# Kernel tuning notes

Measured on AMD Instinct MI355X. Metric: run time of the kernel, lower is better.

Reference implementation:

```python
import jax, jax.numpy as jnp
import numpy as np

HIDDEN = 2048
NUM_HEADS = 16
HEAD_DIM = HIDDEN // NUM_HEADS
INTER = 8192
EPS = 1e-6


def setup_inputs() -> dict:
    key = jax.random.key(0)
    ks = jax.random.split(key, 10)
    s = 0.02
    return {
        "x": jax.random.normal(ks[0], (2, 2048, HIDDEN), dtype=jnp.float32),
        "w_ln1": jnp.ones((HIDDEN,), dtype=jnp.float32),
        "wq": jax.random.normal(ks[1], (HIDDEN, HIDDEN), dtype=jnp.float32) * s,
        "wk": jax.random.normal(ks[2], (HIDDEN, HIDDEN), dtype=jnp.float32) * s,
        "wv": jax.random.normal(ks[3], (HIDDEN, HIDDEN), dtype=jnp.float32) * s,
        "wo": jax.random.normal(ks[4], (HIDDEN, HIDDEN), dtype=jnp.float32) * s,
        "w_ln2": jnp.ones((HIDDEN,), dtype=jnp.float32),
        "wg": jax.random.normal(ks[5], (INTER, HIDDEN), dtype=jnp.float32) * s,
        "wu": jax.random.normal(ks[6], (INTER, HIDDEN), dtype=jnp.float32) * s,
        "wd": jax.random.normal(ks[7], (HIDDEN, INTER), dtype=jnp.float32) * s,
    }


def rmsnorm(x, w):
    rms = jnp.sqrt(jnp.mean(x * x, axis=-1, keepdims=True) + EPS)
    return x / rms * w


def attention(x, wq, wk, wv, wo):
    B, T, C = x.shape
    # weights are [out, in] (torch Linear convention) -> x @ W.T
    q = (x @ wq.T).reshape(B, T, NUM_HEADS, HEAD_DIM)
    k = (x @ wk.T).reshape(B, T, NUM_HEADS, HEAD_DIM)
    v = (x @ wv.T).reshape(B, T, NUM_HEADS, HEAD_DIM)
    scores = jnp.einsum("bqhd,bkhd->bhqk", q, k) / jnp.sqrt(jnp.float32(HEAD_DIM))
    attn = jax.nn.softmax(scores, axis=-1)
    out = jnp.einsum("bhqk,bkhd->bqhd", attn, v).reshape(B, T, C)
    return out @ wo.T


def mlp(x, wg, wu, wd):
    return (jax.nn.silu(x @ wg.T) * (x @ wu.T)) @ wd.T


def reference(x, w_ln1, wq, wk, wv, wo, w_ln2, wg, wu, wd):
    x = x + attention(rmsnorm(x, w_ln1), wq, wk, wv, wo)
    x = x + mlp(rmsnorm(x, w_ln2), wg, wu, wd)
    return x
```

## Files before the change

kernel.cpp:

```cpp
#include <hip/hip_runtime.h>
#include <stdint.h>

typedef unsigned short u16;
typedef unsigned int   u32;
typedef short s16x8 __attribute__((ext_vector_type(8)));
typedef u16   u16x8 __attribute__((ext_vector_type(8)));
typedef float f32x4 __attribute__((ext_vector_type(4)));

__device__ __forceinline__ u16 f2bf(float f) {
    u32 u = __float_as_uint(f);
    u32 r = u + 0x7fffu + ((u >> 16) & 1u);
    return (u16)(r >> 16);
}
__device__ __forceinline__ float bf2f(u16 h) {
    return __uint_as_float(((u32)h) << 16);
}

#define GLD16(gp, lp) __builtin_amdgcn_global_load_lds(                          \
    (const __attribute__((address_space(1))) void*)(uintptr_t)(gp),             \
    (__attribute__((address_space(3))) void*)(u32)(uintptr_t)(lp), 16, 0, 0)

#define FENCE asm volatile("" ::: "memory")

template<int N> __device__ __forceinline__ void waitv() {
    if constexpr (N == 0)      asm volatile("s_waitcnt vmcnt(0)" ::: "memory");
    else if constexpr (N == 3) asm volatile("s_waitcnt vmcnt(3)" ::: "memory");
    else                       asm volatile("s_waitcnt vmcnt(4)" ::: "memory");
}

__global__ __launch_bounds__(256)
void cast_w(const float* __restrict__ in, u16* __restrict__ out, int n)
{
    const int i = (blockIdx.x * 256 + threadIdx.x) * 8;
    if (i >= n) return;
    f32x4 a = *(const f32x4*)(in + i);
    f32x4 b = *(const f32x4*)(in + i + 4);
    u16x8 o;
    o[0] = f2bf(a[0]); o[1] = f2bf(a[1]); o[2] = f2bf(a[2]); o[3] = f2bf(a[3]);
    o[4] = f2bf(b[0]); o[5] = f2bf(b[1]); o[6] = f2bf(b[2]); o[7] = f2bf(b[3]);
    *(u16x8*)(out + i) = o;
}

__global__ __launch_bounds__(256)
void rmsnorm_k(const float* __restrict__ x, const float* __restrict__ wln,
               u16* __restrict__ out, int C)
{
    const int row = blockIdx.x;
    const int tid = threadIdx.x;
    const float* xr = x + (size_t)row * C;
    f32x4 a = *(const f32x4*)(xr + tid * 8);
    f32x4 b = *(const f32x4*)(xr + tid * 8 + 4);
    float s = a[0]*a[0] + a[1]*a[1] + a[2]*a[2] + a[3]*a[3]
            + b[0]*b[0] + b[1]*b[1] + b[2]*b[2] + b[3]*b[3];
    #pragma unroll
    for (int off = 1; off < 64; off <<= 1) s += __shfl_xor(s, off);
    __shared__ float red[4];
    if ((tid & 63) == 0) red[tid >> 6] = s;
    __syncthreads();
    float tot = red[0] + red[1] + red[2] + red[3];
    float inv = rsqrtf(tot / (float)C + 1e-6f);
    f32x4 wa = *(const f32x4*)(wln + tid * 8);
    f32x4 wb = *(const f32x4*)(wln + tid * 8 + 4);
    u16x8 o;
    o[0] = f2bf(a[0]*inv*wa[0]); o[1] = f2bf(a[1]*inv*wa[1]);
    o[2] = f2bf(a[2]*inv*wa[2]); o[3] = f2bf(a[3]*inv*wa[3]);
    o[4] = f2bf(b[0]*inv*wb[0]); o[5] = f2bf(b[1]*inv*wb[1]);
    o[6] = f2bf(b[2]*inv*wb[2]); o[7] = f2bf(b[3]*inv*wb[7-4]);
    *(u16x8*)(out + (size_t)row * C + tid * 8) = o;
}

template<int MODE, int MR>
__global__ __launch_bounds__(512, 1)
void gemm8(const u16* __restrict__ A, const u16* __restrict__ W,
           const float* __restrict__ resid, const u16* __restrict__ aux,
           void* __restrict__ Cout, int M, int N, int K, float scale)
{
    constexpr int BM  = MR * 32;
    constexpr int MR2 = MR / 2;
    constexpr int SRA = MR * 8;
    constexpr int AL  = BM / 128;
    constexpr int WS  = 2 + AL;
    __shared__ __align__(16) u16 lds[2][(BM + 256) * 64];

    const int tid  = threadIdx.x;
    const int lane = tid & 63;
    const int w    = tid >> 6;
    const int wm   = w >> 2;
    const int wn   = w & 3;

    const int gx  = N >> 8;
    const int nwg = gridDim.x;
    const int sid = ((int)blockIdx.x & 7) * (nwg >> 3) + ((int)blockIdx.x >> 3);
    const int brow = (sid / gx) * BM;
    const int bcol = (sid % gx) * 256;

    const int KT = K >> 6;
    const int NI = KT >> 1;

    f32x4 acc[MR][4] = {};

    auto stageA = [&](int buf, int g, int kt) {
        #pragma unroll
        for (int j = 0; j < AL; ++j) {
            const int p   = j * 64 + (tid >> 3);
            const int row = ((p & ~(SRA - 1)) << 1) | (g * SRA) | (p & (SRA - 1));
            const int ch  = (tid & 7) ^ (row & 7);
            const u16* src = A + (size_t)(brow + row) * K + kt * 64 + ch * 8;
            const int p0  = j * 64 + (w << 3);
            const int r0  = ((p0 & ~(SRA - 1)) << 1) | (g * SRA) | (p0 & (SRA - 1));
            GLD16(src, &lds[buf][0] + r0 * 64);
        }
    };
    auto stageB = [&](int buf, int g, int kt) {
        #pragma unroll
        for (int j = 0; j < 2; ++j) {
            const int p   = j * 64 + (tid >> 3);
            const int row = ((p & ~31) << 1) | (g * 32) | (p & 31);
            const int ch  = (tid & 7) ^ (row & 7);
            const u16* src = W + (size_t)(bcol + row) * K + kt * 64 + ch * 8;
            const int p0  = j * 64 + (w << 3);
            const int r0  = ((p0 & ~31) << 1) | (g * 32) | (p0 & 31);
            GLD16(src, &lds[buf][BM * 64] + r0 * 64);
        }
    };

#define LDA(AF, MH, Ab)                                                          \
    _Pragma("unroll") for (int f = 0; f < MR2; ++f)                              \
    _Pragma("unroll") for (int ks = 0; ks < 2; ++ks) {                           \
        const int row = wm * (BM / 2) + (MH) * (BM / 4) + f * 16 + (lane & 15);  \
        const int ch  = (ks * 4 + (lane >> 4)) ^ (row & 7);                      \
        AF[f][ks] = *(const s16x8*)((Ab) + row * 64 + ch * 8);                   \
    }
#define LDB(BQ, NH, Bb)                                                          \
    _Pragma("unroll") for (int g = 0; g < 2; ++g)                                \
    _Pragma("unroll") for (int ks = 0; ks < 2; ++ks) {                           \
        const int row = wn * 64 + (NH) * 32 + g * 16 + (lane & 15);              \
        const int ch  = (ks * 4 + (lane >> 4)) ^ (row & 7);                      \
        BQ[g][ks] = *(const s16x8*)((Bb) + row * 64 + ch * 8);                   \
    }
#define MFQ(AF, BQ, MH, NH)                                                      \
    __builtin_amdgcn_s_setprio(1);                                               \
    _Pragma("unroll") for (int f = 0; f < MR2; ++f)                              \
    _Pragma("unroll") for (int g = 0; g < 2; ++g)                                \
    _Pragma("unroll") for (int ks = 0; ks < 2; ++ks)                             \
        acc[(MH) * MR2 + f][(NH) * 2 + g] =                                      \
            __builtin_amdgcn_mfma_f32_16x16x32_bf16(                             \
                AF[f][ks], BQ[g][ks], acc[(MH) * MR2 + f][(NH) * 2 + g], 0, 0, 0); \
    __builtin_amdgcn_s_setprio(0);
#define BAR1 FENCE; __builtin_amdgcn_s_barrier(); FENCE
#define ENDP asm volatile("s_waitcnt lgkmcnt(0)" ::: "memory");                  \
             FENCE; __builtin_amdgcn_s_barrier(); FENCE

#define KTILE(BUF, S1, S2, S3, S4, W4)                                           \
    {                                                                            \
        const u16* Ab = &lds[BUF][0];                                            \
        const u16* Bb = &lds[BUF][BM * 64];                                      \
        s16x8 afq[MR2][2], bq0[2][2], bq1[2][2];                                 \
        LDA(afq, 0, Ab) LDB(bq0, 0, Bb)                                          \
        S1; BAR1; MFQ(afq, bq0, 0, 0) ENDP;                                      \
        LDB(bq1, 1, Bb)                                                          \
        S2; BAR1; MFQ(afq, bq1, 0, 1) ENDP;                                      \
        LDA(afq, 1, Ab)                                                          \
        S3; BAR1; MFQ(afq, bq1, 1, 1) ENDP;                                      \
        S4; W4; BAR1; MFQ(afq, bq0, 1, 0) ENDP;                                  \
    }

    stageB(0, 0, 0); stageA(0, 1, 0); stageA(0, 0, 0); stageB(0, 1, 0);
    stageB(1, 0, 1); stageA(1, 1, 1);
    waitv<WS>();
    FENCE; __builtin_amdgcn_s_barrier(); FENCE;

    for (int it = 0; it < NI; ++it) {
        const int t1  = 2 * it + 1;
        const int t0n = 2 * it + 2;
        const int t1n = 2 * it + 3;
        const bool s0 = t0n < KT, s1 = t1n < KT;
        const bool last = (it == NI - 1);

        KTILE(0,
              { stageB(1, 1, t1); },
              { stageA(1, 0, t1); },
              { if (s0) stageB(0, 0, t0n); },
              { if (s0) stageA(0, 1, t0n); },
              { if (last) waitv<0>(); else waitv<WS>(); })
        KTILE(1,
              { if (s0) stageA(0, 0, t0n); },
              { if (s0) stageB(0, 1, t0n); },
              { if (s1) stageB(1, 0, t1n); },
              { if (s1) stageA(1, 1, t1n); },
              { if (!last) waitv<WS>(); })
    }
#undef KTILE
#undef LDA
#undef LDB
#undef MFQ
#undef BAR1
#undef ENDP

    const int er = (lane >> 4) * 4;
    const int ec = lane & 15;
    #pragma unroll
    for (int i = 0; i < MR; ++i) {
        #pragma unroll
        for (int j = 0; j < 4; ++j) {
            #pragma unroll
            for (int r = 0; r < 4; ++r) {
                const int row = brow + wm * (BM / 2) + i * 16 + er + r;
                const int col = bcol + wn * 64 + j * 16 + ec;
                const size_t idx = (size_t)row * N + col;
                const float va = acc[i][j][r];
                if (MODE == 0)      ((u16*)Cout)[idx] = f2bf(va);
                else if (MODE == 1) ((u16*)Cout)[idx] = f2bf(va * scale);
                else if (MODE == 2) ((float*)Cout)[idx] = resid[idx] + va;
                else {
                    const float g  = bf2f(aux[idx]);
                    const float sg = g / (1.0f + exp2f(-g * 1.4426950408889634f));
                    ((u16*)Cout)[idx] = f2bf(sg * va);
                }
            }
        }
    }
}

__global__ __launch_bounds__(512, 1)
void flash_attn(const u16* __restrict__ q, const u16* __restrict__ k,
                const u16* __restrict__ vT, u16* __restrict__ o)
{
    __shared__ __align__(16) u16 Kt[2][64 * 128];
    __shared__ __align__(16) u16 Vt[2][128 * 64];
    __shared__ __align__(16) u16 Pw[8][32 * 64];
    const int tid  = threadIdx.x;
    const int lane = tid & 63;
    const int w    = tid >> 6;
    const int qtile = blockIdx.x;
    const int bh    = blockIdx.y;
    const int b = bh >> 4, h = bh & 15;
    const size_t head  = ((size_t)b * 2048) * 2048 + (size_t)h * 128;
    const size_t vbase = ((size_t)h * 128) * 4096 + (size_t)b * 2048;

    s16x8 qf[2][4];
    #pragma unroll
    for (int qi = 0; qi < 2; ++qi) {
        const int tq = qtile * 256 + w * 32 + qi * 16 + (lane & 15);
        const u16* qp = q + head + (size_t)tq * 2048 + (lane >> 4) * 8;
        #pragma unroll
        for (int dk = 0; dk < 4; ++dk) qf[qi][dk] = *(const s16x8*)(qp + dk * 32);
    }

    f32x4 oa[2][8] = {};
    float m_r[2][4] = {{-1e30f,-1e30f,-1e30f,-1e30f},{-1e30f,-1e30f,-1e30f,-1e30f}};
    float l_r[2][4] = {};

    const int krow = tid >> 3;
    const int kcol = (tid & 7) * 16;
    const int vd   = tid >> 2;
    const int vk   = (tid & 3) * 16;
    const u16* kg = k + head + (size_t)krow * 2048 + kcol;
    const u16* vg = vT + vbase + (size_t)vd * 4096 + vk;
    const u32 kw0 = (u32)((krow * 256 + kcol * 2)      ^ ((krow & 7) << 4));
    const u32 kw1 = (u32)((krow * 256 + kcol * 2 + 16) ^ ((krow & 7) << 4));
    const u32 vw0 = (u32)((vd * 128 + vk * 2)          ^ ((vd & 7) << 4));
    const u32 vw1 = (u32)((vd * 128 + vk * 2 + 16)     ^ ((vd & 7) << 4));

    char* PwB = (char*)&Pw[w][0];

    s16x8 kr0 = *(const s16x8*)(kg);
    s16x8 kr1 = *(const s16x8*)(kg + 8);
    s16x8 vr0 = *(const s16x8*)(vg);
    s16x8 vr1 = *(const s16x8*)(vg + 8);

    for (int kb = 0; kb < 32; ++kb) {
        const int cur = kb & 1;
        char* KtB = (char*)&Kt[cur][0];
        char* VtB = (char*)&Vt[cur][0];
        *(s16x8*)(KtB + kw0) = kr0;
        *(s16x8*)(KtB + kw1) = kr1;
        *(s16x8*)(VtB + vw0) = vr0;
        *(s16x8*)(VtB + vw1) = vr1;
        if (kb + 1 < 32) {
            const int k0n = (kb + 1) * 64;
            kr0 = *(const s16x8*)(kg + (size_t)k0n * 2048);
            kr1 = *(const s16x8*)(kg + (size_t)k0n * 2048 + 8);
            vr0 = *(const s16x8*)(vg + k0n);
            vr1 = *(const s16x8*)(vg + k0n + 8);
        }
        asm volatile("s_waitcnt lgkmcnt(0)" ::: "memory");
        __builtin_amdgcn_s_barrier();
        FENCE;

        f32x4 s[2][4] = {};
        __builtin_amdgcn_s_setprio(1);
        #pragma unroll
        for (int kt = 0; kt < 4; ++kt) {
            const int row = kt * 16 + (lane & 15);
            s16x8 kf[4];
            #pragma unroll
            for (int dk = 0; dk < 4; ++dk) {
                const int dcol = dk * 32 + (lane >> 4) * 8;
                kf[dk] = *(const s16x8*)(KtB + ((row * 256 + dcol * 2) ^ ((row & 7) << 4)));
            }
            #pragma unroll
            for (int qi = 0; qi < 2; ++qi)
                #pragma unroll
                for (int dk = 0; dk < 4; ++dk)
                    s[qi][kt] = __builtin_amdgcn_mfma_f32_16x16x32_bf16(qf[qi][dk], kf[dk], s[qi][kt], 0, 0, 0);
        }
        __builtin_amdgcn_s_setprio(0);

        #pragma unroll
        for (int qi = 0; qi < 2; ++qi) {
            float mx[4];
            #pragma unroll
            for (int r = 0; r < 4; ++r) {
                float m0 = fmaxf(fmaxf(s[qi][0][r], s[qi][1][r]), fmaxf(s[qi][2][r], s[qi][3][r]));
                m0 = fmaxf(m0, __shfl_xor(m0, 1));
                m0 = fmaxf(m0, __shfl_xor(m0, 2));
                m0 = fmaxf(m0, __shfl_xor(m0, 4));
                m0 = fmaxf(m0, __shfl_xor(m0, 8));
                mx[r] = m0;
            }
            const bool grow = (mx[0] > m_r[qi][0] + 8.f) || (mx[1] > m_r[qi][1] + 8.f) ||
                              (mx[2] > m_r[qi][2] + 8.f) || (mx[3] > m_r[qi][3] + 8.f);
            if (__any(grow)) {
                #pragma unroll
                for (int r = 0; r < 4; ++r) {
                    const float mn = fmaxf(m_r[qi][r], mx[r]);
                    const float sc = exp2f(m_r[qi][r] - mn);
                    m_r[qi][r] = mn;
                    l_r[qi][r] *= sc;
                    #pragma unroll
                    for (int ni = 0; ni < 8; ++ni) oa[qi][ni][r] *= sc;
                }
            }
            #pragma unroll
            for (int r = 0; r < 4; ++r) {
                const float p0 = exp2f(s[qi][0][r] - m_r[qi][r]);
                const float p1 = exp2f(s[qi][1][r] - m_r[qi][r]);
                const float p2 = exp2f(s[qi][2][r] - m_r[qi][r]);
                const float p3 = exp2f(s[qi][3][r] - m_r[qi][r]);
                s[qi][0][r] = p0; s[qi][1][r] = p1; s[qi][2][r] = p2; s[qi][3][r] = p3;
                float sum = p0 + p1 + p2 + p3;
                sum += __shfl_xor(sum, 1);
                sum += __shfl_xor(sum, 2);
                sum += __shfl_xor(sum, 4);
                sum += __shfl_xor(sum, 8);
                l_r[qi][r] += sum;
            }
            #pragma unroll
            for (int kt = 0; kt < 4; ++kt) {
                const int kc = kt * 16 + (lane & 15);
                #pragma unroll
                for (int r = 0; r < 4; ++r) {
                    const int qr = qi * 16 + (lane >> 4) * 4 + r;
                    *(u16*)(PwB + ((qr * 128 + kc * 2) ^ (((qr >> 2) & 3) << 5))) = f2bf(s[qi][kt][r]);
                }
            }
        }
        __builtin_amdgcn_s_setprio(1);
        #pragma unroll
        for (int kt2 = 0; kt2 < 2; ++kt2) {
            const int keyb = kt2 * 32 + (lane >> 4) * 8;
            s16x8 pf[2];
            #pragma unroll
            for (int qi = 0; qi < 2; ++qi) {
                const int qrow = qi * 16 + (lane & 15);
                pf[qi] = *(const s16x8*)(PwB + ((qrow * 128 + keyb * 2) ^ (((qrow >> 2) & 3) << 5)));
            }
            #pragma unroll
            for (int ni = 0; ni < 8; ++ni) {
                const int dd = ni * 16 + (lane & 15);
                s16x8 vf = *(const s16x8*)(VtB + ((dd * 128 + keyb * 2) ^ ((dd & 7) << 4)));
                #pragma unroll
                for (int qi = 0; qi < 2; ++qi)
                    oa[qi][ni] = __builtin_amdgcn_mfma_f32_16x16x32_bf16(pf[qi], vf, oa[qi][ni], 0, 0, 0);
            }
        }
        __builtin_amdgcn_s_setprio(0);
    }
    #pragma unroll
    for (int qi = 0; qi < 2; ++qi) {
        #pragma unroll
        for (int r = 0; r < 4; ++r) {
            const float inv = 1.0f / l_r[qi][r];
            const int tout = qtile * 256 + w * 32 + qi * 16 + (lane >> 4) * 4 + r;
            u16* op = o + head + (size_t)tout * 2048 + (lane & 15);
            #pragma unroll
            for (int ni = 0; ni < 8; ++ni)
                op[ni * 16] = f2bf(oa[qi][ni][r] * inv);
        }
    }
}

extern "C" void kernel_launch(void* const* d_in, const int* in_sizes, int n_in,
                              void* d_out, int out_size, void* d_ws, size_t ws_size,
                              hipStream_t stream)
{
    (void)in_sizes; (void)n_in; (void)out_size; (void)ws_size;
    const float* x    = (const float*)d_in[0];
    const float* wln1 = (const float*)d_in[1];
    const float* wq   = (const float*)d_in[2];
    const float* wk   = (const float*)d_in[3];
    const float* wv   = (const float*)d_in[4];
    const float* wo   = (const float*)d_in[5];
    const float* wln2 = (const float*)d_in[6];
    const float* wg   = (const float*)d_in[7];
    const float* wu   = (const float*)d_in[8];
    const float* wd   = (const float*)d_in[9];
    float* out = (float*)d_out;

    const size_t MB = 1024ull * 1024ull;
    char* ws = (char*)d_ws;
    u16*   arena = (u16*)(ws + 0);
    float* hbuf  = (float*)(ws + 32 * MB);
    u16*   xn    = (u16*)(ws + 64 * MB);
    u16*   qb    = (u16*)(ws + 80 * MB);
    u16*   kbuf  = (u16*)(ws + 96 * MB);
    u16*   vT    = (u16*)(ws + 112 * MB);
    u16*   abuf  = (u16*)(ws + 128 * MB);
    u16*   gbuf  = (u16*)(ws + 80 * MB);

    const int M = 4096, C = 2048, I = 8192;
    const float qscale = 0.1275164899f;
    dim3 blk(256);
    dim3 blk8(512);

    rmsnorm_k<<<M, blk, 0, stream>>>(x, wln1, xn, C);

    cast_w<<<(C * C) / 2048, blk, 0, stream>>>(wq, arena, C * C);
    gemm8<1, 4><<<dim3((C / 256) * (M / 128)), blk8, 0, stream>>>(xn, arena, nullptr, nullptr, qb, M, C, C, qscale);
    cast_w<<<(C * C) / 2048, blk, 0, stream>>>(wk, arena, C * C);
    gemm8<0, 4><<<dim3((C / 256) * (M / 128)), blk8, 0, stream>>>(xn, arena, nullptr, nullptr, kbuf, M, C, C, 1.f);
    cast_w<<<(C * C) / 2048, blk, 0, stream>>>(wv, arena, C * C);
    gemm8<0, 4><<<dim3((M / 256) * (C / 128)), blk8, 0, stream>>>(arena, xn, nullptr, nullptr, vT, C, M, C, 1.f);

    flash_attn<<<dim3(2048 / 256, 32), blk8, 0, stream>>>(qb, kbuf, vT, abuf);

    cast_w<<<(C * C) / 2048, blk, 0, stream>>>(wo, arena, C * C);
    gemm8<2, 4><<<dim3((C / 256) * (M / 128)), blk8, 0, stream>>>(abuf, arena, x, nullptr, hbuf, M, C, C, 1.f);

    rmsnorm_k<<<M, blk, 0, stream>>>(hbuf, wln2, xn, C);

    cast_w<<<(I * C) / 2048, blk, 0, stream>>>(wg, arena, I * C);
    gemm8<0, 8><<<dim3((I / 256) * (M / 256)), blk8, 0, stream>>>(xn, arena, nullptr, nullptr, gbuf, M, I, C, 1.f);
    cast_w<<<(I * C) / 2048, blk, 0, stream>>>(wu, arena, I * C);
    gemm8<3, 8><<<dim3((I / 256) * (M / 256)), blk8, 0, stream>>>(xn, arena, nullptr, gbuf, gbuf, M, I, C, 1.f);
    cast_w<<<(C * I) / 2048, blk, 0, stream>>>(wd, arena, C * I);
    gemm8<2, 4><<<dim3((C / 256) * (M / 128)), blk8, 0, stream>>>(gbuf, arena, hbuf, nullptr, out, M, C, I, 1.f);
}
```

Before: 754.7 us.

## Keep softmax probabilities in registers via transposed QK^T and permlane swaps

The attention kernel now computes S transposed (K as the A operand), so each lane holds one query row. The row max and sum reductions then take two cross-lane shuffles instead of four per row. Probabilities are packed to bf16 with v_cvt_pk_bf16_f32 and rearranged into the PV MFMA operand layout with permlane32/16 swaps, removing the per-wave LDS scratch buffer and its scattered 2-byte stores. With that buffer gone, launch bounds ask for two blocks per CU, which adds register pressure risk; the rmsnorm index expression is also tidied.

Measured after the change: 718.9 us. -4.7%, faster.

```diff
diff --git a/kernel.cpp b/kernel.cpp
--- a/kernel.cpp
+++ b/kernel.cpp
@@ -5,6 +5,7 @@
 typedef unsigned int   u32;
 typedef short s16x8 __attribute__((ext_vector_type(8)));
 typedef u16   u16x8 __attribute__((ext_vector_type(8)));
+typedef u32   u32x4 __attribute__((ext_vector_type(4)));
 typedef float f32x4 __attribute__((ext_vector_type(4)));
 
 __device__ __forceinline__ u16 f2bf(float f) {
@@ -14,6 +15,28 @@
 }
 __device__ __forceinline__ float bf2f(u16 h) {
     return __uint_as_float(((u32)h) << 16);
+}
+
+__device__ __forceinline__ u32 cvtpk(float a, float b) {
+    u32 r;
+    asm("v_cvt_pk_bf16_f32 %0, %1, %2" : "=v"(r) : "v"(a), "v"(b));
+    return r;
+}
+__device__ __forceinline__ void swap32(u32& a, u32& b) {
+#if __has_builtin(__builtin_amdgcn_permlane32_swap)
+    auto r = __builtin_amdgcn_permlane32_swap(a, b, false, false);
+    a = r[0]; b = r[1];
+#else
+    asm volatile("v_permlane32_swap_b32 %0, %1" : "+v"(a), "+v"(b));
+#endif
+}
+__device__ __forceinline__ void swap16(u32& a, u32& b) {
+#if __has_builtin(__builtin_amdgcn_permlane16_swap)
+    auto r = __builtin_amdgcn_permlane16_swap(a, b, false, false);
+    a = r[0]; b = r[1];
+#else
+    asm volatile("v_permlane16_swap_b32 %0, %1" : "+v"(a), "+v"(b));
+#endif
 }
 
 #define GLD16(gp, lp) __builtin_amdgcn_global_load_lds(                          \
@@ -65,7 +88,7 @@
     o[0] = f2bf(a[0]*inv*wa[0]); o[1] = f2bf(a[1]*inv*wa[1]);
     o[2] = f2bf(a[2]*inv*wa[2]); o[3] = f2bf(a[3]*inv*wa[3]);
     o[4] = f2bf(b[0]*inv*wb[0]); o[5] = f2bf(b[1]*inv*wb[1]);
-    o[6] = f2bf(b[2]*inv*wb[2]); o[7] = f2bf(b[3]*inv*wb[7-4]);
+    o[6] = f2bf(b[2]*inv*wb[2]); o[7] = f2bf(b[3]*inv*wb[3]);
     *(u16x8*)(out + (size_t)row * C + tid * 8) = o;
 }
 
@@ -222,13 +245,12 @@
     }
 }
 
-__global__ __launch_bounds__(512, 1)
+__global__ __launch_bounds__(512, 2)
 void flash_attn(const u16* __restrict__ q, const u16* __restrict__ k,
                 const u16* __restrict__ vT, u16* __restrict__ o)
 {
     __shared__ __align__(16) u16 Kt[2][64 * 128];
     __shared__ __align__(16) u16 Vt[2][128 * 64];
-    __shared__ __align__(16) u16 Pw[8][32 * 64];
     const int tid  = threadIdx.x;
     const int lane = tid & 63;
     const int w    = tid >> 6;
@@ -248,8 +270,8 @@
     }
 
     f32x4 oa[2][8] = {};
-    float m_r[2][4] = {{-1e30f,-1e30f,-1e30f,-1e30f},{-1e30f,-1e30f,-1e30f,-1e30f}};
-    float l_r[2][4] = {};
+    float m_r[2] = {-1e30f, -1e30f};
+    float l_r[2] = {0.f, 0.f};
 
     const int krow = tid >> 3;
     const int kcol = (tid & 7) * 16;
@@ -261,8 +283,6 @@
     const u32 kw1 = (u32)((krow * 256 + kcol * 2 + 16) ^ ((krow & 7) << 4));
     const u32 vw0 = (u32)((vd * 128 + vk * 2)          ^ ((vd & 7) << 4));
     const u32 vw1 = (u32)((vd * 128 + vk * 2 + 16)     ^ ((vd & 7) << 4));
-
-    char* PwB = (char*)&Pw[w][0];
 
     s16x8 kr0 = *(const s16x8*)(kg);
     s16x8 kr1 = *(const s16x8*)(kg + 8);
@@ -288,7 +308,7 @@
         __builtin_amdgcn_s_barrier();
         FENCE;
 
-        f32x4 s[2][4] = {};
+        f32x4 st[2][4] = {};
         __builtin_amdgcn_s_setprio(1);
         #pragma unroll
         for (int kt = 0; kt < 4; ++kt) {
@@ -303,76 +323,86 @@
             for (int qi = 0; qi < 2; ++qi)
                 #pragma unroll
                 for (int dk = 0; dk < 4; ++dk)
-                    s[qi][kt] = __builtin_amdgcn_mfma_f32_16x16x32_bf16(qf[qi][dk], kf[dk], s[qi][kt], 0, 0, 0);
+                    st[qi][kt] = __builtin_amdgcn_mfma_f32_16x16x32_bf16(kf[dk], qf[qi][dk], st[qi][kt], 0, 0, 0);
         }
         __builtin_amdgcn_s_setprio(0);
 
+        float mx[2];
         #pragma unroll
         for (int qi = 0; qi < 2; ++qi) {
-            float mx[4];
-            #pragma unroll
-            for (int r = 0; r < 4; ++r) {
-                float m0 = fmaxf(fmaxf(s[qi][0][r], s[qi][1][r]), fmaxf(s[qi][2][r], s[qi][3][r]));
-                m0 = fmaxf(m0, __shfl_xor(m0, 1));
-                m0 = fmaxf(m0, __shfl_xor(m0, 2));
-                m0 = fmaxf(m0, __shfl_xor(m0, 4));
-                m0 = fmaxf(m0, __shfl_xor(m0, 8));
-                mx[r] = m0;
-            }
-            const bool grow = (mx[0] > m_r[qi][0] + 8.f) || (mx[1] > m_r[qi][1] + 8.f) ||
-                              (mx[2] > m_r[qi][2] + 8.f) || (mx[3] > m_r[qi][3] + 8.f);
-            if (__any(grow)) {
+            float m0 = fmaxf(fmaxf(st[qi][0][0], st[qi][0][1]), fmaxf(st[qi][0][2], st[qi][0][3]));
+            float m1 = fmaxf(fmaxf(st[qi][1][0], st[qi][1][1]), fmaxf(st[qi][1][2], st[qi][1][3]));
+            float m2 = fmaxf(fmaxf(st[qi][2][0], st[qi][2][1]), fmaxf(st[qi][2][2], st[qi][2][3]));
+            float m3 = fmaxf(fmaxf(st[qi][3][0], st[qi][3][1]), fmaxf(st[qi][3][2], st[qi][3][3]));
+            float m0123 = fmaxf(fmaxf(m0, m1), fmaxf(m2, m3));
+            m0123 = fmaxf(m0123, __shfl_xor(m0123, 16));
+            m0123 = fmaxf(m0123, __shfl_xor(m0123, 32));
+            mx[qi] = m0123;
+        }
+        const bool grow = (mx[0] > m_r[0] + 8.f) || (mx[1] > m_r[1] + 8.f);
+        if (__any(grow)) {
+            #pragma unroll
+            for (int qi = 0; qi < 2; ++qi) {
+                const float mn = fmaxf(m_r[qi], mx[qi]);
+                const float sc = exp2f(m_r[qi] - mn);
+                m_r[qi] = mn;
+                l_r[qi] *= sc;
+                const float s0 = __shfl(sc, (lane >> 4) * 4 + 0);
+                const float s1 = __shfl(sc, (lane >> 4) * 4 + 1);
+                const float s2 = __shfl(sc, (lane >> 4) * 4 + 2);
+                const float s3 = __shfl(sc, (lane >> 4) * 4 + 3);
+                #pragma unroll
+                for (int ni = 0; ni < 8; ++ni) {
+                    oa[qi][ni][0] *= s0; oa[qi][ni][1] *= s1;
+                    oa[qi][ni][2] *= s2; oa[qi][ni][3] *= s3;
+                }
+            }
+        }
+
+        s16x8 pa[2][2];
+        #pragma unroll
+        for (int qi = 0; qi < 2; ++qi) {
+            float sum = 0.f;
+            #pragma unroll
+            for (int kt = 0; kt < 4; ++kt)
                 #pragma unroll
                 for (int r = 0; r < 4; ++r) {
-                    const float mn = fmaxf(m_r[qi][r], mx[r]);
-                    const float sc = exp2f(m_r[qi][r] - mn);
-                    m_r[qi][r] = mn;
-                    l_r[qi][r] *= sc;
-                    #pragma unroll
-                    for (int ni = 0; ni < 8; ++ni) oa[qi][ni][r] *= sc;
+                    const float p = exp2f(st[qi][kt][r] - m_r[qi]);
+                    st[qi][kt][r] = p;
+                    sum += p;
                 }
-            }
-            #pragma unroll
-            for (int r = 0; r < 4; ++r) {
-                const float p0 = exp2f(s[qi][0][r] - m_r[qi][r]);
-                const float p1 = exp2f(s[qi][1][r] - m_r[qi][r]);
-                const float p2 = exp2f(s[qi][2][r] - m_r[qi][r]);
-                const float p3 = exp2f(s[qi][3][r] - m_r[qi][r]);
-                s[qi][0][r] = p0; s[qi][1][r] = p1; s[qi][2][r] = p2; s[qi][3][r] = p3;
-                float sum = p0 + p1 + p2 + p3;
-                sum += __shfl_xor(sum, 1);
-                sum += __shfl_xor(sum, 2);
-                sum += __shfl_xor(sum, 4);
-                sum += __shfl_xor(sum, 8);
-                l_r[qi][r] += sum;
-            }
+            sum += __shfl_xor(sum, 16);
+            sum += __shfl_xor(sum, 32);
+            l_r[qi] += sum;
+
+            u32 q01[4], q23[4];
             #pragma unroll
             for (int kt = 0; kt < 4; ++kt) {
-                const int kc = kt * 16 + (lane & 15);
-                #pragma unroll
-                for (int r = 0; r < 4; ++r) {
-                    const int qr = qi * 16 + (lane >> 4) * 4 + r;
-                    *(u16*)(PwB + ((qr * 128 + kc * 2) ^ (((qr >> 2) & 3) << 5))) = f2bf(s[qi][kt][r]);
-                }
-            }
-        }
+                q01[kt] = cvtpk(st[qi][kt][0], st[qi][kt][1]);
+                q23[kt] = cvtpk(st[qi][kt][2], st[qi][kt][3]);
+            }
+            #pragma unroll
+            for (int ks = 0; ks < 2; ++ks) {
+                u32 X = q01[2 * ks], Y = q01[2 * ks + 1];
+                swap32(X, Y); swap16(X, Y);
+                u32 U = q23[2 * ks], V = q23[2 * ks + 1];
+                swap32(U, V); swap16(U, V);
+                u32x4 t; t[0] = X; t[1] = U; t[2] = Y; t[3] = V;
+                pa[qi][ks] = __builtin_bit_cast(s16x8, t);
+            }
+        }
+
         __builtin_amdgcn_s_setprio(1);
         #pragma unroll
-        for (int kt2 = 0; kt2 < 2; ++kt2) {
-            const int keyb = kt2 * 32 + (lane >> 4) * 8;
-            s16x8 pf[2];
-            #pragma unroll
-            for (int qi = 0; qi < 2; ++qi) {
-                const int qrow = qi * 16 + (lane & 15);
-                pf[qi] = *(const s16x8*)(PwB + ((qrow * 128 + keyb * 2) ^ (((qrow >> 2) & 3) << 5)));
-            }
+        for (int ks = 0; ks < 2; ++ks) {
+            const int keyb = ks * 32 + (lane >> 4) * 8;
             #pragma unroll
             for (int ni = 0; ni < 8; ++ni) {
                 const int dd = ni * 16 + (lane & 15);
                 s16x8 vf = *(const s16x8*)(VtB + ((dd * 128 + keyb * 2) ^ ((dd & 7) << 4)));
                 #pragma unroll
                 for (int qi = 0; qi < 2; ++qi)
-                    oa[qi][ni] = __builtin_amdgcn_mfma_f32_16x16x32_bf16(pf[qi], vf, oa[qi][ni], 0, 0, 0);
+                    oa[qi][ni] = __builtin_amdgcn_mfma_f32_16x16x32_bf16(pa[qi][ks], vf, oa[qi][ni], 0, 0, 0);
             }
         }
         __builtin_amdgcn_s_setprio(0);
@@ -381,7 +411,7 @@
     for (int qi = 0; qi < 2; ++qi) {
         #pragma unroll
         for (int r = 0; r < 4; ++r) {
-            const float inv = 1.0f / l_r[qi][r];
+            const float inv = 1.0f / __shfl(l_r[qi], (lane >> 4) * 4 + r);
             const int tout = qtile * 256 + w * 32 + qi * 16 + (lane >> 4) * 4 + r;
             u16* op = o + head + (size_t)tout * 2048 + (lane & 15);
             #pragma unroll
```
